# Kernel optimization log

Hardware: AMD Instinct MI355X
Metric: run time of the kernel (lower is better)

## Reference

```python
import jax, jax.numpy as jnp
import numpy as np

N_NODES = 100000
N_EDGES = 400000
D = 128

def _mlp_ln(x, W1, b1, W2, b2, W3, b3, gamma, beta):
    h = jax.nn.relu(x @ W1 + b1)
    h = jax.nn.relu(h @ W2 + b2)
    h = h @ W3 + b3
    mu = jnp.mean(h, axis=-1, keepdims=True)
    var = jnp.var(h, axis=-1, keepdims=True)
    return (h - mu) * jax.lax.rsqrt(var + 1e-5) * gamma + beta


def setup_inputs() -> dict:
    key = jax.random.key(0)
    ks = jax.random.split(key, 12)
    s = lambda fan_in: 1.0 / np.sqrt(fan_in)
    inp = {
        'node_features': jax.random.normal(ks[0], (1, N_NODES, D), jnp.float32),
        'edge_features': jax.random.normal(ks[1], (1, N_EDGES, D), jnp.float32),
        'senders': jax.random.randint(ks[2], (1, N_EDGES), 0, N_NODES, jnp.int32),
        'receivers': jax.random.randint(ks[3], (1, N_EDGES), 0, N_NODES, jnp.int32),
        'e_W1': jax.random.normal(ks[4], (3 * D, D), jnp.float32) * s(3 * D),
        'e_b1': jnp.zeros((D,), jnp.float32),
        'e_W2': jax.random.normal(ks[5], (D, D), jnp.float32) * s(D),
        'e_b2': jnp.zeros((D,), jnp.float32),
        'e_W3': jax.random.normal(ks[6], (D, D), jnp.float32) * s(D),
        'e_b3': jnp.zeros((D,), jnp.float32),
        'e_gamma': jnp.ones((D,), jnp.float32),
        'e_beta': jnp.zeros((D,), jnp.float32),
        'n_W1': jax.random.normal(ks[7], (2 * D, D), jnp.float32) * s(2 * D),
        'n_b1': jnp.zeros((D,), jnp.float32),
        'n_W2': jax.random.normal(ks[8], (D, D), jnp.float32) * s(D),
        'n_b2': jnp.zeros((D,), jnp.float32),
        'n_W3': jax.random.normal(ks[9], (D, D), jnp.float32) * s(D),
        'n_b3': jnp.zeros((D,), jnp.float32),
        'n_gamma': jnp.ones((D,), jnp.float32),
        'n_beta': jnp.zeros((D,), jnp.float32),
    }
    return inp


def reference(node_features, edge_features, senders, receivers,
              e_W1, e_b1, e_W2, e_b2, e_W3, e_b3, e_gamma, e_beta,
              n_W1, n_b1, n_W2, n_b2, n_W3, n_b3, n_gamma, n_beta):
    # batch dim is 1; indexing matches torch.index_select(dim=1, senders[0])
    snd = senders[0]
    rcv = receivers[0]
    nodes = node_features[0]          # [N, D]
    edges = edge_features[0]          # [E, D]

    # edge update: gather, concat, edge MLP
    edge_in = jnp.concatenate([nodes[snd], nodes[rcv], edges], axis=-1)  # [E, 3D]
    new_edges = _mlp_ln(edge_in, e_W1, e_b1, e_W2, e_b2, e_W3, e_b3, e_gamma, e_beta)

    # node update: segment-sum aggregate to receivers, concat, node MLP
    agg = jax.ops.segment_sum(new_edges, rcv, num_segments=nodes.shape[0])  # [N, D]
    node_in = jnp.concatenate([nodes, agg], axis=-1)                        # [N, 2D]
    new_nodes = _mlp_ln(node_in, n_W1, n_b1, n_W2, n_b2, n_W3, n_b3, n_gamma, n_beta)

    # residuals
    new_nodes = new_nodes + nodes
    new_edges = new_edges + edges
    return new_nodes[None], new_edges[None]
```

## Files before the change

kernel.cpp:

```cpp
#include <hip/hip_runtime.h>
#include <stdint.h>

#define NNODES 100000
#define NEDGES 400000
#define DD 128

typedef __attribute__((ext_vector_type(4))) float f32x4;
typedef __attribute__((ext_vector_type(8))) short bf16x8;

__device__ __forceinline__ short f2b(float x){
  union { float f; uint32_t u; } v; v.f = x;
  uint32_t r = v.u + 0x7FFFu + ((v.u >> 16) & 1u);
  return (short)(r >> 16);
}

__device__ __forceinline__ bf16x8 pack_bf8(f32x4 a, f32x4 b){
  bf16x8 r;
  r[0]=f2b(a[0]); r[1]=f2b(a[1]); r[2]=f2b(a[2]); r[3]=f2b(a[3]);
  r[4]=f2b(b[0]); r[5]=f2b(b[1]); r[6]=f2b(b[2]); r[7]=f2b(b[3]);
  return r;
}

__global__ void pack_w_kernel(const float* __restrict__ W, short* __restrict__ dst, int total){
  int o = blockIdx.x*256 + threadIdx.x;
  if (o >= total) return;
  int kt = o >> 12, rem = o & 4095;
  int g = rem >> 10, n = (rem >> 3) & 127, j = rem & 7;
  int k = kt*32 + g*8 + j;
  dst[o] = f2b(W[k*DD + n]);
}

template<int MODE>
__global__ __launch_bounds__(256, 2) void gnb_mlp(
    const float* __restrict__ nodef, const float* __restrict__ edgef,
    const int* __restrict__ snd, const int* __restrict__ rcv,
    const short* __restrict__ Wp1, const short* __restrict__ Wp2, const short* __restrict__ Wp3,
    const float* __restrict__ b1p, const float* __restrict__ b2p, const float* __restrict__ b3p,
    const float* __restrict__ gmp, const float* __restrict__ btp,
    float* __restrict__ agg, float* __restrict__ outp, int nrows)
{
  constexpr int KT1 = (MODE==0) ? 12 : 8;
  __shared__ __align__(16) short Ws[4096];
  __shared__ __align__(16) short Hs[8192];

  const int tid  = threadIdx.x;
  const int lane = tid & 63;
  const int wid  = tid >> 6;
  const int l16  = lane & 15;
  const int hi   = lane >> 4;
  const int row0 = blockIdx.x * 64;
  const int arow_l = wid*16 + l16;
  const int arow_g = row0 + arow_l;
  const int arow_c = (arow_g < nrows) ? arow_g : (nrows-1);

  int sidx = 0, ridx = 0;
  if (MODE==0){ sidx = snd[arow_c]; ridx = rcv[arow_c]; }

  f32x4 acc[8];
  #pragma unroll
  for (int t=0;t<8;t++) acc[t] = (f32x4)(0.0f);

  #pragma unroll
  for (int kt=0; kt<KT1; kt++){
    const int4* ws_src = (const int4*)(Wp1 + kt*4096);
    int4 w0 = ws_src[tid]; int4 w1 = ws_src[tid+256];
    __syncthreads();
    ((int4*)Ws)[tid] = w0; ((int4*)Ws)[tid+256] = w1;
    __syncthreads();

    const float* s;
    if (MODE==0){
      s = (kt<4) ? (nodef + (size_t)sidx*DD)
        : (kt<8) ? (nodef + (size_t)ridx*DD)
                 : (edgef + (size_t)arow_c*DD);
    } else {
      s = (kt<4) ? (nodef + (size_t)arow_c*DD) : (agg + (size_t)arow_c*DD);
    }
    const int ko = (kt&3)*32 + hi*8;
    f32x4 x0 = *(const f32x4*)(s+ko);
    f32x4 x1 = *(const f32x4*)(s+ko+4);
    bf16x8 af = pack_bf8(x0,x1);
    #pragma unroll
    for (int t=0;t<8;t++){
      bf16x8 bw = *(const bf16x8*)&Ws[hi*1024 + (t*16+l16)*8];
      acc[t] = __builtin_amdgcn_mfma_f32_16x16x32_bf16(af, bw, acc[t], 0,0,0);
    }
  }
  #pragma unroll
  for (int t=0;t<8;t++){
    const float bb = b1p[t*16+l16];
    const int col2 = (t*16+l16)*2;
    #pragma unroll
    for (int r=0;r<4;r++){
      float v = fmaxf(acc[t][r] + bb, 0.0f);
      int row = wid*16 + hi*4 + r;
      *(short*)((char*)Hs + row*256 + (col2 ^ ((row&7)<<4))) = f2b(v);
      acc[t][r] = 0.0f;
    }
  }

  #pragma unroll
  for (int L=0; L<2; L++){
    const short* Wp = (L==0) ? Wp2 : Wp3;
    #pragma unroll
    for (int kt=0; kt<4; kt++){
      const int4* ws_src = (const int4*)(Wp + kt*4096);
      int4 w0 = ws_src[tid]; int4 w1 = ws_src[tid+256];
      __syncthreads();
      ((int4*)Ws)[tid] = w0; ((int4*)Ws)[tid+256] = w1;
      __syncthreads();
      bf16x8 af = *(const bf16x8*)((char*)Hs + arow_l*256 + ((kt*64 + hi*16) ^ ((arow_l&7)<<4)));
      #pragma unroll
      for (int t=0;t<8;t++){
        bf16x8 bw = *(const bf16x8*)&Ws[hi*1024 + (t*16+l16)*8];
        acc[t] = __builtin_amdgcn_mfma_f32_16x16x32_bf16(af, bw, acc[t], 0,0,0);
      }
    }
    if (L==0){
      #pragma unroll
      for (int t=0;t<8;t++){
        const float bb = b2p[t*16+l16];
        const int col2 = (t*16+l16)*2;
        #pragma unroll
        for (int r=0;r<4;r++){
          float v = fmaxf(acc[t][r] + bb, 0.0f);
          int row = wid*16 + hi*4 + r;
          *(short*)((char*)Hs + row*256 + (col2 ^ ((row&7)<<4))) = f2b(v);
          acc[t][r] = 0.0f;
        }
      }
    }
  }

  float ps[4] = {0,0,0,0}, pq[4] = {0,0,0,0};
  #pragma unroll
  for (int t=0;t<8;t++){
    const float bb = b3p[t*16+l16];
    #pragma unroll
    for (int r=0;r<4;r++){
      float v = acc[t][r] + bb;
      acc[t][r] = v;
      ps[r] += v; pq[r] += v*v;
    }
  }
  #pragma unroll
  for (int m=1;m<16;m<<=1){
    #pragma unroll
    for (int r=0;r<4;r++){
      ps[r] += __shfl_xor(ps[r], m);
      pq[r] += __shfl_xor(pq[r], m);
    }
  }
  float mu[4], rs[4];
  #pragma unroll
  for (int r=0;r<4;r++){
    mu[r] = ps[r] * (1.0f/128.0f);
    float var = pq[r] * (1.0f/128.0f) - mu[r]*mu[r];
    rs[r] = rsqrtf(var + 1e-5f);
  }

  int erow[4]; int rdst[4] = {0,0,0,0};
  #pragma unroll
  for (int r=0;r<4;r++){
    erow[r] = row0 + wid*16 + hi*4 + r;
    if (MODE==0) rdst[r] = rcv[erow[r]];
  }

  #pragma unroll
  for (int t=0;t<8;t++){
    const int col = t*16+l16;
    const float g = gmp[col], be = btp[col];
    #pragma unroll
    for (int r=0;r<4;r++){
      float y = (acc[t][r]-mu[r])*rs[r]*g + be;
      if (MODE==0){
        size_t o = (size_t)erow[r]*DD + col;
        outp[o] = y + edgef[o];
        atomicAdd(agg + (size_t)rdst[r]*DD + col, y);
      } else {
        if (erow[r] < nrows){
          size_t o = (size_t)erow[r]*DD + col;
          outp[o] = y + nodef[o];
        }
      }
    }
  }
}

extern "C" void kernel_launch(void* const* d_in, const int* in_sizes, int n_in,
                              void* d_out, int out_size, void* d_ws, size_t ws_size,
                              hipStream_t stream)
{
  (void)in_sizes; (void)n_in; (void)out_size; (void)ws_size;
  const float* nodef = (const float*)d_in[0];
  const float* edgef = (const float*)d_in[1];
  const int*   snd   = (const int*)d_in[2];
  const int*   rcv   = (const int*)d_in[3];
  const float* eW1 = (const float*)d_in[4];
  const float* eb1 = (const float*)d_in[5];
  const float* eW2 = (const float*)d_in[6];
  const float* eb2 = (const float*)d_in[7];
  const float* eW3 = (const float*)d_in[8];
  const float* eb3 = (const float*)d_in[9];
  const float* egm = (const float*)d_in[10];
  const float* ebt = (const float*)d_in[11];
  const float* nW1 = (const float*)d_in[12];
  const float* nb1 = (const float*)d_in[13];
  const float* nW2 = (const float*)d_in[14];
  const float* nb2 = (const float*)d_in[15];
  const float* nW3 = (const float*)d_in[16];
  const float* nb3 = (const float*)d_in[17];
  const float* ngm = (const float*)d_in[18];
  const float* nbt = (const float*)d_in[19];

  float* agg = (float*)d_ws;
  short* wp  = (short*)((char*)d_ws + (size_t)NNODES*DD*sizeof(float));
  short* we1 = wp;
  short* we2 = wp + 49152;
  short* we3 = wp + 65536;
  short* wn1 = wp + 81920;
  short* wn2 = wp + 114688;
  short* wn3 = wp + 131072;

  hipMemsetAsync(agg, 0, (size_t)NNODES*DD*sizeof(float), stream);
  pack_w_kernel<<<192,256,0,stream>>>(eW1, we1, 49152);
  pack_w_kernel<<<64, 256,0,stream>>>(eW2, we2, 16384);
  pack_w_kernel<<<64, 256,0,stream>>>(eW3, we3, 16384);
  pack_w_kernel<<<128,256,0,stream>>>(nW1, wn1, 32768);
  pack_w_kernel<<<64, 256,0,stream>>>(nW2, wn2, 16384);
  pack_w_kernel<<<64, 256,0,stream>>>(nW3, wn3, 16384);

  float* out_nodes = (float*)d_out;
  float* out_edges = out_nodes + (size_t)NNODES*DD;

  gnb_mlp<0><<<NEDGES/64, 256, 0, stream>>>(nodef, edgef, snd, rcv,
      we1, we2, we3, eb1, eb2, eb3, egm, ebt, agg, out_edges, NEDGES);
  gnb_mlp<1><<<(NNODES+63)/64, 256, 0, stream>>>(nodef, edgef, snd, rcv,
      wn1, wn2, wn3, nb1, nb2, nb3, ngm, nbt, agg, out_nodes, NNODES);
}
```

Baseline: 424.7 us.

## Precompute per-node first-layer projections and gather them instead of raw node features

Uses linearity of the first MLP layer: node features are projected once per node through the sender, receiver and node-side slices of W1 into a bf16 table. The edge kernel then gathers and sums the two projected rows instead of doing a 384-wide matmul per edge. The node kernel reuses the same table for its node half. Blocks grow to 512 threads and 128 rows, with whole weight matrices staged in LDS and the next layer's weights prefetched, and the six pack kernels become one launch. The cost is an extra kernel, a 77MB bf16 intermediate table, and extra bf16 rounding of the pre-activation sums.

```diff
diff --git a/kernel.cpp b/kernel.cpp
--- a/kernel.cpp
+++ b/kernel.cpp
@@ -3,7 +3,6 @@
 
 #define NNODES 100000
 #define NEDGES 400000
-#define DD 128
 
 typedef __attribute__((ext_vector_type(4))) float f32x4;
 typedef __attribute__((ext_vector_type(8))) short bf16x8;
@@ -13,7 +12,9 @@
   uint32_t r = v.u + 0x7FFFu + ((v.u >> 16) & 1u);
   return (short)(r >> 16);
 }
-
+__device__ __forceinline__ float b2f(short x){
+  union { uint32_t u; float f; } v; v.u = ((uint32_t)(unsigned short)x) << 16; return v.f;
+}
 __device__ __forceinline__ bf16x8 pack_bf8(f32x4 a, f32x4 b){
   bf16x8 r;
   r[0]=f2b(a[0]); r[1]=f2b(a[1]); r[2]=f2b(a[2]); r[3]=f2b(a[3]);
@@ -21,121 +22,206 @@
   return r;
 }
 
-__global__ void pack_w_kernel(const float* __restrict__ W, short* __restrict__ dst, int total){
+__global__ void pack_all(const float* __restrict__ eW1, const float* __restrict__ eW2,
+                         const float* __restrict__ eW3, const float* __restrict__ nW1,
+                         const float* __restrict__ nW2, const float* __restrict__ nW3,
+                         short* __restrict__ dst){
   int o = blockIdx.x*256 + threadIdx.x;
-  if (o >= total) return;
-  int kt = o >> 12, rem = o & 4095;
-  int g = rem >> 10, n = (rem >> 3) & 127, j = rem & 7;
+  int seg = o >> 14, rem = o & 16383;
+  int kt = rem >> 12, g = (rem >> 10) & 3, n = (rem >> 3) & 127, j = rem & 7;
   int k = kt*32 + g*8 + j;
-  dst[o] = f2b(W[k*DD + n]);
+  const float* src = eW1; int koff = 0;
+  switch(seg){
+    case 0: src=eW1; koff=0;   break;
+    case 1: src=eW1; koff=128; break;
+    case 2: src=nW1; koff=0;   break;
+    case 3: src=eW1; koff=256; break;
+    case 4: src=nW1; koff=128; break;
+    case 5: src=eW2; break;
+    case 6: src=eW3; break;
+    case 7: src=nW2; break;
+    case 8: src=nW3; break;
+  }
+  dst[o] = f2b(src[(size_t)(koff+k)*128 + n]);
+}
+
+__global__ __launch_bounds__(512,4) void compute_T(
+    const float* __restrict__ nodef, const short* __restrict__ wp,
+    short* __restrict__ Tt, int nrows)
+{
+  __shared__ __align__(16) short Ws[16384];
+  const int tid=threadIdx.x, lane=tid&63, wid=tid>>6, l16=lane&15, hi=lane>>4;
+  const int row0 = blockIdx.x*128;
+  const int arow_l = wid*16 + l16;
+  const int arow_c = min(row0 + arow_l, nrows-1);
+  const float* s = nodef + (size_t)arow_c*128;
+
+  bf16x8 af[4];
+  #pragma unroll
+  for (int kt=0; kt<4; kt++){
+    int ko = kt*32 + hi*8;
+    af[kt] = pack_bf8(*(const f32x4*)(s+ko), *(const f32x4*)(s+ko+4));
+  }
+  int4 w[4];
+  #pragma unroll
+  for (int i=0;i<4;i++) w[i] = ((const int4*)wp)[tid + 512*i];
+
+  for (int o=0; o<3; o++){
+    if (o) __syncthreads();
+    #pragma unroll
+    for (int i=0;i<4;i++) ((int4*)Ws)[tid + 512*i] = w[i];
+    if (o < 2){
+      #pragma unroll
+      for (int i=0;i<4;i++) w[i] = ((const int4*)(wp + (o+1)*16384))[tid + 512*i];
+    }
+    __syncthreads();
+    f32x4 acc[8];
+    #pragma unroll
+    for (int t=0;t<8;t++) acc[t] = (f32x4)(0.0f);
+    #pragma unroll
+    for (int kt=0;kt<4;kt++){
+      #pragma unroll
+      for (int t=0;t<8;t++){
+        bf16x8 bw = *(const bf16x8*)&Ws[kt*4096 + hi*1024 + (t*16+l16)*8];
+        acc[t] = __builtin_amdgcn_mfma_f32_16x16x32_bf16(af[kt], bw, acc[t], 0,0,0);
+      }
+    }
+    #pragma unroll
+    for (int t=0;t<8;t++){
+      int col = t*16 + l16;
+      #pragma unroll
+      for (int r=0;r<4;r++){
+        int row = row0 + wid*16 + hi*4 + r;
+        if (row < nrows) Tt[(size_t)row*384 + o*128 + col] = f2b(acc[t][r]);
+      }
+    }
+  }
 }
 
 template<int MODE>
-__global__ __launch_bounds__(256, 2) void gnb_mlp(
+__global__ __launch_bounds__(512,4) void gnb_mlp(
     const float* __restrict__ nodef, const float* __restrict__ edgef,
     const int* __restrict__ snd, const int* __restrict__ rcv,
+    const short* __restrict__ Tt,
     const short* __restrict__ Wp1, const short* __restrict__ Wp2, const short* __restrict__ Wp3,
     const float* __restrict__ b1p, const float* __restrict__ b2p, const float* __restrict__ b3p,
     const float* __restrict__ gmp, const float* __restrict__ btp,
     float* __restrict__ agg, float* __restrict__ outp, int nrows)
 {
-  constexpr int KT1 = (MODE==0) ? 12 : 8;
-  __shared__ __align__(16) short Ws[4096];
-  __shared__ __align__(16) short Hs[8192];
-
-  const int tid  = threadIdx.x;
-  const int lane = tid & 63;
-  const int wid  = tid >> 6;
-  const int l16  = lane & 15;
-  const int hi   = lane >> 4;
-  const int row0 = blockIdx.x * 64;
+  __shared__ __align__(16) short Ws[16384];
+  __shared__ __align__(16) short HGs[16384];
+
+  const int tid=threadIdx.x, lane=tid&63, wid=tid>>6, l16=lane&15, hi=lane>>4;
+  const int row0 = blockIdx.x*128;
   const int arow_l = wid*16 + l16;
-  const int arow_g = row0 + arow_l;
-  const int arow_c = (arow_g < nrows) ? arow_g : (nrows-1);
-
-  int sidx = 0, ridx = 0;
-  if (MODE==0){ sidx = snd[arow_c]; ridx = rcv[arow_c]; }
+  const int arow_c = min(row0 + arow_l, nrows-1);
+
+  int4 w[4];
+  #pragma unroll
+  for (int i=0;i<4;i++) w[i] = ((const int4*)Wp1)[tid + 512*i];
+
+  if (MODE==0){
+    #pragma unroll
+    for (int u=0;u<4;u++){
+      int q = tid + u*512;
+      int gr = q >> 4, c = q & 15;
+      int grow = row0 + gr;
+      int si = snd[grow], ri = rcv[grow];
+      bf16x8 a = *(const bf16x8*)(Tt + (size_t)si*384 + c*8);
+      bf16x8 b = *(const bf16x8*)(Tt + (size_t)ri*384 + 128 + c*8);
+      bf16x8 o8;
+      #pragma unroll
+      for (int j=0;j<8;j++) o8[j] = f2b(b2f(a[j]) + b2f(b[j]));
+      *(bf16x8*)((char*)HGs + gr*256 + ((c*16) ^ ((gr&7)<<4))) = o8;
+    }
+  }
+  #pragma unroll
+  for (int i=0;i<4;i++) ((int4*)Ws)[tid + 512*i] = w[i];
+  #pragma unroll
+  for (int i=0;i<4;i++) w[i] = ((const int4*)Wp2)[tid + 512*i];
+  __syncthreads();
 
   f32x4 acc[8];
   #pragma unroll
   for (int t=0;t<8;t++) acc[t] = (f32x4)(0.0f);
 
-  #pragma unroll
-  for (int kt=0; kt<KT1; kt++){
-    const int4* ws_src = (const int4*)(Wp1 + kt*4096);
-    int4 w0 = ws_src[tid]; int4 w1 = ws_src[tid+256];
-    __syncthreads();
-    ((int4*)Ws)[tid] = w0; ((int4*)Ws)[tid+256] = w1;
-    __syncthreads();
-
-    const float* s;
-    if (MODE==0){
-      s = (kt<4) ? (nodef + (size_t)sidx*DD)
-        : (kt<8) ? (nodef + (size_t)ridx*DD)
-                 : (edgef + (size_t)arow_c*DD);
-    } else {
-      s = (kt<4) ? (nodef + (size_t)arow_c*DD) : (agg + (size_t)arow_c*DD);
-    }
-    const int ko = (kt&3)*32 + hi*8;
-    f32x4 x0 = *(const f32x4*)(s+ko);
-    f32x4 x1 = *(const f32x4*)(s+ko+4);
-    bf16x8 af = pack_bf8(x0,x1);
+  const float* s1 = (MODE==0) ? (edgef + (size_t)arow_c*128) : (agg + (size_t)arow_c*128);
+  #pragma unroll
+  for (int kt=0;kt<4;kt++){
+    int ko = kt*32 + hi*8;
+    bf16x8 af = pack_bf8(*(const f32x4*)(s1+ko), *(const f32x4*)(s1+ko+4));
     #pragma unroll
     for (int t=0;t<8;t++){
-      bf16x8 bw = *(const bf16x8*)&Ws[hi*1024 + (t*16+l16)*8];
+      bf16x8 bw = *(const bf16x8*)&Ws[kt*4096 + hi*1024 + (t*16+l16)*8];
       acc[t] = __builtin_amdgcn_mfma_f32_16x16x32_bf16(af, bw, acc[t], 0,0,0);
     }
   }
   #pragma unroll
   for (int t=0;t<8;t++){
-    const float bb = b1p[t*16+l16];
-    const int col2 = (t*16+l16)*2;
+    int col = t*16 + l16;
+    float bb = b1p[col];
+    #pragma unroll
+    for (int r=0;r<4;r++){
+      int row = wid*16 + hi*4 + r;
+      float g;
+      if (MODE==0){
+        g = b2f(*(const short*)((char*)HGs + row*256 + ((col*2) ^ ((row&7)<<4))));
+      } else {
+        int grow = min(row0 + row, nrows-1);
+        g = b2f(Tt[(size_t)grow*384 + 256 + col]);
+      }
+      float v = fmaxf(acc[t][r] + g + bb, 0.0f);
+      *(short*)((char*)HGs + row*256 + ((col*2) ^ ((row&7)<<4))) = f2b(v);
+      acc[t][r] = 0.0f;
+    }
+  }
+  __syncthreads();
+  #pragma unroll
+  for (int i=0;i<4;i++) ((int4*)Ws)[tid + 512*i] = w[i];
+  #pragma unroll
+  for (int i=0;i<4;i++) w[i] = ((const int4*)Wp3)[tid + 512*i];
+  __syncthreads();
+
+  #pragma unroll
+  for (int kt=0;kt<4;kt++){
+    bf16x8 af = *(const bf16x8*)((char*)HGs + arow_l*256 + ((kt*64 + hi*16) ^ ((arow_l&7)<<4)));
+    #pragma unroll
+    for (int t=0;t<8;t++){
+      bf16x8 bw = *(const bf16x8*)&Ws[kt*4096 + hi*1024 + (t*16+l16)*8];
+      acc[t] = __builtin_amdgcn_mfma_f32_16x16x32_bf16(af, bw, acc[t], 0,0,0);
+    }
+  }
+  #pragma unroll
+  for (int t=0;t<8;t++){
+    float bb = b2p[t*16+l16];
+    int col2 = (t*16+l16)*2;
     #pragma unroll
     for (int r=0;r<4;r++){
       float v = fmaxf(acc[t][r] + bb, 0.0f);
       int row = wid*16 + hi*4 + r;
-      *(short*)((char*)Hs + row*256 + (col2 ^ ((row&7)<<4))) = f2b(v);
+      *(short*)((char*)HGs + row*256 + (col2 ^ ((row&7)<<4))) = f2b(v);
       acc[t][r] = 0.0f;
     }
   }
-
-  #pragma unroll
-  for (int L=0; L<2; L++){
-    const short* Wp = (L==0) ? Wp2 : Wp3;
-    #pragma unroll
-    for (int kt=0; kt<4; kt++){
-      const int4* ws_src = (const int4*)(Wp + kt*4096);
-      int4 w0 = ws_src[tid]; int4 w1 = ws_src[tid+256];
-      __syncthreads();
-      ((int4*)Ws)[tid] = w0; ((int4*)Ws)[tid+256] = w1;
-      __syncthreads();
-      bf16x8 af = *(const bf16x8*)((char*)Hs + arow_l*256 + ((kt*64 + hi*16) ^ ((arow_l&7)<<4)));
-      #pragma unroll
-      for (int t=0;t<8;t++){
-        bf16x8 bw = *(const bf16x8*)&Ws[hi*1024 + (t*16+l16)*8];
-        acc[t] = __builtin_amdgcn_mfma_f32_16x16x32_bf16(af, bw, acc[t], 0,0,0);
-      }
-    }
-    if (L==0){
-      #pragma unroll
-      for (int t=0;t<8;t++){
-        const float bb = b2p[t*16+l16];
-        const int col2 = (t*16+l16)*2;
-        #pragma unroll
-        for (int r=0;r<4;r++){
-          float v = fmaxf(acc[t][r] + bb, 0.0f);
-          int row = wid*16 + hi*4 + r;
-          *(short*)((char*)Hs + row*256 + (col2 ^ ((row&7)<<4))) = f2b(v);
-          acc[t][r] = 0.0f;
-        }
-      }
+  __syncthreads();
+  #pragma unroll
+  for (int i=0;i<4;i++) ((int4*)Ws)[tid + 512*i] = w[i];
+  __syncthreads();
+
+  #pragma unroll
+  for (int kt=0;kt<4;kt++){
+    bf16x8 af = *(const bf16x8*)((char*)HGs + arow_l*256 + ((kt*64 + hi*16) ^ ((arow_l&7)<<4)));
+    #pragma unroll
+    for (int t=0;t<8;t++){
+      bf16x8 bw = *(const bf16x8*)&Ws[kt*4096 + hi*1024 + (t*16+l16)*8];
+      acc[t] = __builtin_amdgcn_mfma_f32_16x16x32_bf16(af, bw, acc[t], 0,0,0);
     }
   }
 
   float ps[4] = {0,0,0,0}, pq[4] = {0,0,0,0};
   #pragma unroll
   for (int t=0;t<8;t++){
-    const float bb = b3p[t*16+l16];
+    float bb = b3p[t*16+l16];
     #pragma unroll
     for (int r=0;r<4;r++){
       float v = acc[t][r] + bb;
@@ -168,18 +254,18 @@
 
   #pragma unroll
   for (int t=0;t<8;t++){
-    const int col = t*16+l16;
-    const float g = gmp[col], be = btp[col];
-    #pragma unroll
-    for (int r=0;r<4;r++){
-      float y = (acc[t][r]-mu[r])*rs[r]*g + be;
+    int col = t*16 + l16;
+    float gm = gmp[col], be = btp[col];
+    #pragma unroll
+    for (int r=0;r<4;r++){
+      float y = (acc[t][r]-mu[r])*rs[r]*gm + be;
       if (MODE==0){
-        size_t o = (size_t)erow[r]*DD + col;
+        size_t o = (size_t)erow[r]*128 + col;
         outp[o] = y + edgef[o];
-        atomicAdd(agg + (size_t)rdst[r]*DD + col, y);
+        atomicAdd(agg + (size_t)rdst[r]*128 + col, y);
       } else {
         if (erow[r] < nrows){
-          size_t o = (size_t)erow[r]*DD + col;
+          size_t o = (size_t)erow[r]*128 + col;
           outp[o] = y + nodef[o];
         }
       }
@@ -214,27 +300,19 @@
   const float* nbt = (const float*)d_in[19];
 
   float* agg = (float*)d_ws;
-  short* wp  = (short*)((char*)d_ws + (size_t)NNODES*DD*sizeof(float));
-  short* we1 = wp;
-  short* we2 = wp + 49152;
-  short* we3 = wp + 65536;
-  short* wn1 = wp + 81920;
-  short* wn2 = wp + 114688;
-  short* wn3 = wp + 131072;
-
-  hipMemsetAsync(agg, 0, (size_t)NNODES*DD*sizeof(float), stream);
-  pack_w_kernel<<<192,256,0,stream>>>(eW1, we1, 49152);
-  pack_w_kernel<<<64, 256,0,stream>>>(eW2, we2, 16384);
-  pack_w_kernel<<<64, 256,0,stream>>>(eW3, we3, 16384);
-  pack_w_kernel<<<128,256,0,stream>>>(nW1, wn1, 32768);
-  pack_w_kernel<<<64, 256,0,stream>>>(nW2, wn2, 16384);
-  pack_w_kernel<<<64, 256,0,stream>>>(nW3, wn3, 16384);
+  short* Tt  = (short*)((char*)d_ws + (size_t)NNODES*128*4);
+  short* wp  = (short*)((char*)d_ws + (size_t)NNODES*128*4
+                                    + (size_t)NNODES*384*2);
+
+  hipMemsetAsync(agg, 0, (size_t)NNODES*128*4, stream);
+  pack_all<<<576,256,0,stream>>>(eW1,eW2,eW3,nW1,nW2,nW3,wp);
+  compute_T<<<(NNODES+127)/128,512,0,stream>>>(nodef, wp, Tt, NNODES);
 
   float* out_nodes = (float*)d_out;
-  float* out_edges = out_nodes + (size_t)NNODES*DD;
-
-  gnb_mlp<0><<<NEDGES/64, 256, 0, stream>>>(nodef, edgef, snd, rcv,
-      we1, we2, we3, eb1, eb2, eb3, egm, ebt, agg, out_edges, NEDGES);
-  gnb_mlp<1><<<(NNODES+63)/64, 256, 0, stream>>>(nodef, edgef, snd, rcv,
-      wn1, wn2, wn3, nb1, nb2, nb3, ngm, nbt, agg, out_nodes, NNODES);
-}
+  float* out_edges = out_nodes + (size_t)NNODES*128;
+
+  gnb_mlp<0><<<NEDGES/128,512,0,stream>>>(nodef, edgef, snd, rcv, Tt,
+      wp+3*16384, wp+5*16384, wp+6*16384, eb1,eb2,eb3, egm,ebt, agg, out_edges, NEDGES);
+  gnb_mlp<1><<<(NNODES+127)/128,512,0,stream>>>(nodef, edgef, snd, rcv, Tt,
+      wp+4*16384, wp+7*16384, wp+8*16384, nb1,nb2,nb3, ngm,nbt, agg, out_nodes, NNODES);
+}
```

New measurement: 523.8 us. 23.3% more time.
